# Kernel tuning notes

Measured on AMD Instinct MI355X. Metric: run time of the kernel, lower is better.

The kernel has to match this reference:

```python
import jax, jax.numpy as jnp
import numpy as np

B, L, W = 64, 20, 48
D = W * W           # 2304, MoE input/output size (image_width**2)
E = 4               # num_experts
HID = 2 * D         # expert hidden size
K = 1               # top_k
LOSS_COEF = 1e-2


def _cv_squared(x):
    # torch: x.var() (unbiased) / (x.mean()**2 + eps)
    eps = 1e-10
    return jnp.var(x, ddof=1) / (jnp.mean(x) ** 2 + eps)


def _moe(x, w_gate, w1, b1, w2, b2):
    # Noisy top-k gating, inference path (train=False => clean logits, no noise).
    logits = x @ w_gate                                   # [B, E]
    top_logits, top_idx = jax.lax.top_k(logits, K + 1)    # min(k+1, E)
    topk_gates = jax.nn.softmax(top_logits[:, :K], axis=-1)
    gates = jnp.zeros_like(logits).at[
        jnp.arange(x.shape[0])[:, None], top_idx[:, :K]
    ].set(topk_gates)                                     # [B, E] sparse gates
    importance = gates.sum(0)
    load = (gates > 0).sum(0).astype(x.dtype)             # _gates_to_load
    aux = LOSS_COEF * (_cv_squared(importance) + _cv_squared(load))
    # Dense expert compute weighted by gates (same math as dispatch/combine).
    h = jax.nn.relu(jnp.einsum('bd,edh->beh', x, w1) + b1)      # [B,E,HID]
    y = jnp.einsum('beh,ehd->bed', h, w2) + b2                  # [B,E,D]
    out = jnp.einsum('be,bed->bd', gates, y)                    # [B,D]
    return out, aux


def _conv3d(x, w, b, pad):
    y = jax.lax.conv_general_dilated(
        x, w, window_strides=(1, 1, 1), padding=pad,
        dimension_numbers=('NCDHW', 'OIDHW', 'NCDHW'))
    return y + b[None, :, None, None, None]


def _forward(input, conv1_w, conv1_b, conv2_w, conv2_b,
             t_gate, t_w1, t_b1, t_w2, t_b2,
             a_gate, a_w1, a_b1, a_w2, a_b2,
             q_gate, q_w1, q_b1, q_w2, q_b2,
             enc_w, enc_b, dec_w, dec_b):
    x = jnp.transpose(input, (0, 2, 1, 3, 4))                   # [B,1,L,H,W]
    x = jax.nn.relu(_conv3d(x, conv1_w, conv1_b, ((1, 1), (1, 1), (1, 1))))
    x = jax.nn.relu(_conv3d(x, conv2_w, conv2_b, ((0, 0), (1, 1), (1, 1))))  # [B,1,1,H,W]
    xf = x.reshape(x.shape[0], -1)                              # [B, D]
    transform, l1 = _moe(xf, t_gate, t_w1, t_b1, t_w2, t_b2)
    add, l2 = _moe(xf, a_gate, a_w1, a_b1, a_w2, a_b2)
    quad, l3 = _moe(xf, q_gate, q_w1, q_b1, q_w2, q_b2)
    s = input.shape                                             # [B,L,1,H,W]
    transform = transform.reshape(s[0], 1, s[2], s[3], s[4])
    add = add.reshape(s[0], 1, s[2], s[3], s[4])
    quad = quad.reshape(s[0], 1, s[2], s[3], s[4])
    out = input * input * quad + input * transform + add        # [B,L,1,H,W]
    # encoder = Linear(D,D)+ReLU, decoder = Linear(D,D) over flattened H*W
    of = out.reshape(s[0], s[1], D)
    of = jax.nn.relu(of @ enc_w + enc_b)
    of = of @ dec_w + dec_b
    of = jax.nn.sigmoid(of)
    return of.reshape(s), l1 + l2 + l3


def setup_inputs() -> dict:
    key = jax.random.key(0)
    ks = jax.random.split(key, 32)
    sc = 0.02
    inp = {
        'input': jax.random.normal(ks[0], (B, L, 1, W, W), jnp.float32),
        'conv1_w': jax.random.normal(ks[1], (10, 1, 3, 3, 3), jnp.float32) * sc,
        'conv1_b': jnp.zeros((10,), jnp.float32),
        'conv2_w': jax.random.normal(ks[2], (1, 10, L, 3, 3), jnp.float32) * sc,
        'conv2_b': jnp.zeros((1,), jnp.float32),
        'enc_w': jax.random.normal(ks[3], (D, D), jnp.float32) * sc,
        'enc_b': jnp.zeros((D,), jnp.float32),
        'dec_w': jax.random.normal(ks[4], (D, D), jnp.float32) * sc,
        'dec_b': jnp.zeros((D,), jnp.float32),
    }
    for i, p in enumerate(['t', 'a', 'q']):
        k0, k1, k2 = jax.random.split(ks[5 + i], 3)
        inp[p + '_gate'] = jnp.zeros((D, E), jnp.float32) + jax.random.normal(k0, (D, E), jnp.float32) * sc
        inp[p + '_w1'] = jax.random.normal(k1, (E, D, HID), jnp.float32) * sc
        inp[p + '_b1'] = jnp.zeros((E, HID), jnp.float32)
        inp[p + '_w2'] = jax.random.normal(k2, (E, HID, D), jnp.float32) * sc
        inp[p + '_b2'] = jnp.zeros((E, D), jnp.float32)
    return inp


def reference(input, conv1_w, conv1_b, conv2_w, conv2_b,
              t_gate, t_w1, t_b1, t_w2, t_b2,
              a_gate, a_w1, a_b1, a_w2, a_b2,
              q_gate, q_w1, q_b1, q_w2, q_b2,
              enc_w, enc_b, dec_w, dec_b):
    return _forward(input, conv1_w, conv1_b, conv2_w, conv2_b,
                    t_gate, t_w1, t_b1, t_w2, t_b2,
                    a_gate, a_w1, a_b1, a_w2, a_b2,
                    q_gate, q_w1, q_b1, q_w2, q_b2,
                    enc_w, enc_b, dec_w, dec_b)
```

## Files before the change

### kernel.cpp

```cpp
#include <hip/hip_runtime.h>
#include <stdint.h>

#define NB 64
#define NL 20
#define ND 2304
#define NE 4
#define NH 4608
#define NM 1280

typedef float f32x4 __attribute__((ext_vector_type(4)));
typedef __bf16 bf16x8 __attribute__((ext_vector_type(8)));
typedef unsigned short u16;
typedef u16 u16x4 __attribute__((ext_vector_type(4)));
typedef unsigned int u32;
typedef u32 u32x4 __attribute__((ext_vector_type(4)));

__device__ __forceinline__ u16 f2bf(float f) {
  u32 u = __builtin_bit_cast(u32, f);
  u += 0x7fffu + ((u >> 16) & 1u);
  return (u16)(u >> 16);
}

__device__ __forceinline__ void gl_lds16(const void* g, void* l) {
  __builtin_amdgcn_global_load_lds(
      (const __attribute__((address_space(1))) void*)g,
      (__attribute__((address_space(3))) void*)l, 16, 0, 0);
}

#define OFF_XFACC 0
#define OFF_XF    147456
#define OFF_H     294912
#define OFF_Y     1179648
#define OFF_AUX   1622016
#define OFF_CNT   1622020
#define OFF_ROWS  1622032
#define OFF_OFB   1622240
#define OFF_H1B   3096800
#define OFF_ENCWB 4571360
#define OFF_DECWB 7225568
#define OFF_XC    9879776
#define OFF_P     10322144

__global__ __launch_bounds__(256) void k_zero(float* __restrict__ p) {
  p[(size_t)blockIdx.x * 256 + threadIdx.x] = 0.f;
}

__global__ __launch_bounds__(256) void k_conv(
    const float* __restrict__ in, const float* __restrict__ w1,
    const float* __restrict__ b1, const float* __restrict__ w2,
    float* __restrict__ xf_acc) {
  __shared__ float insl[3][50][50];
  __shared__ float c1[2][50][50];
  __shared__ float w1s[270];
  __shared__ float w2s[90];
  __shared__ float b1s[10];
  const int d = blockIdx.x, b = blockIdx.y, t = threadIdx.x;
  for (int i = t; i < 270; i += 256) w1s[i] = w1[i];
  for (int i = t; i < 90; i += 256) w2s[i] = w2[(size_t)((i / 9) * 20 + d) * 9 + (i % 9)];
  if (t < 10) b1s[t] = b1[t];
  for (int i = t; i < 7500; i += 256) {
    int s = i / 2500, rr = (i % 2500) / 50, cc = i % 50;
    int gd = d - 1 + s, gy = rr - 1, gx = cc - 1;
    float v = 0.f;
    if (gd >= 0 && gd < NL && (unsigned)gy < 48u && (unsigned)gx < 48u)
      v = in[((size_t)b * NL + gd) * ND + gy * 48 + gx];
    insl[s][rr][cc] = v;
  }
  for (int i = t; i < 5000; i += 256) ((float*)c1)[i] = 0.f;
  float s2[3][4];
#pragma unroll
  for (int qi = 0; qi < 3; ++qi)
#pragma unroll
    for (int xq = 0; xq < 4; ++xq) s2[qi][xq] = 0.f;
  __syncthreads();
  for (int pc = 0; pc < 5; ++pc) {
#pragma unroll
    for (int qi = 0; qi < 3; ++qi) {
      int q = t + qi * 256;
      if (q < 576) {
        int y = q / 12, x0 = (q % 12) * 4;
        float a0[4], a1[4];
        const float bb0 = b1s[2 * pc], bb1 = b1s[2 * pc + 1];
#pragma unroll
        for (int xq = 0; xq < 4; ++xq) { a0[xq] = bb0; a1[xq] = bb1; }
#pragma unroll
        for (int kd = 0; kd < 3; ++kd)
#pragma unroll
          for (int ky = 0; ky < 3; ++ky) {
            float v[6];
#pragma unroll
            for (int i = 0; i < 6; ++i) v[i] = insl[kd][y + ky][x0 + i];
            const float* wa = &w1s[(2 * pc) * 27 + kd * 9 + ky * 3];
            const float* wb = wa + 27;
#pragma unroll
            for (int xq = 0; xq < 4; ++xq) {
              a0[xq] += v[xq] * wa[0] + v[xq + 1] * wa[1] + v[xq + 2] * wa[2];
              a1[xq] += v[xq] * wb[0] + v[xq + 1] * wb[1] + v[xq + 2] * wb[2];
            }
          }
#pragma unroll
        for (int xq = 0; xq < 4; ++xq) {
          c1[0][y + 1][x0 + 1 + xq] = fmaxf(a0[xq], 0.f);
          c1[1][y + 1][x0 + 1 + xq] = fmaxf(a1[xq], 0.f);
        }
      }
    }
    __syncthreads();
#pragma unroll
    for (int qi = 0; qi < 3; ++qi) {
      int q = t + qi * 256;
      if (q < 576) {
        int y = q / 12, x0 = (q % 12) * 4;
#pragma unroll
        for (int cc = 0; cc < 2; ++cc) {
#pragma unroll
          for (int ky = 0; ky < 3; ++ky) {
            float v[6];
#pragma unroll
            for (int i = 0; i < 6; ++i) v[i] = c1[cc][y + ky][x0 + i];
            const float* wr = &w2s[(2 * pc + cc) * 9 + ky * 3];
#pragma unroll
            for (int xq = 0; xq < 4; ++xq)
              s2[qi][xq] += v[xq] * wr[0] + v[xq + 1] * wr[1] + v[xq + 2] * wr[2];
          }
        }
      }
    }
    __syncthreads();
  }
#pragma unroll
  for (int qi = 0; qi < 3; ++qi) {
    int q = t + qi * 256;
    if (q < 576) {
#pragma unroll
      for (int xq = 0; xq < 4; ++xq)
        atomicAdd(&xf_acc[(size_t)b * ND + q * 4 + xq], s2[qi][xq]);
    }
  }
}

__global__ __launch_bounds__(256) void k_bias_relu(
    const float* __restrict__ acc, const float* __restrict__ c2b, float* __restrict__ xf) {
  size_t i = (size_t)blockIdx.x * 256 + threadIdx.x;
  xf[i] = fmaxf(acc[i] + c2b[0], 0.f);
}

__global__ __launch_bounds__(256) void k_gate(
    const float* __restrict__ xf,
    const float* __restrict__ g0, const float* __restrict__ g1, const float* __restrict__ g2,
    float* __restrict__ aux, int* __restrict__ cnt, int* __restrict__ rows) {
  const int p = blockIdx.x, t = threadIdx.x;
  const float* __restrict__ g = (p == 0) ? g0 : ((p == 1) ? g1 : g2);
  __shared__ float lg[64][4];
  __shared__ int lidx[64];
  __shared__ int lcnt[4];
  if (t < 4) lcnt[t] = 0;
  const int wv = t >> 6, l = t & 63;
  for (int b0 = 0; b0 < 64; b0 += 4) {
    int bb = b0 + wv;
    f32x4 acc = {0.f, 0.f, 0.f, 0.f};
    const float* xr = xf + (size_t)bb * ND + l * 36;
    const float* gr = g + (size_t)l * 36 * 4;
#pragma unroll
    for (int i4 = 0; i4 < 9; ++i4) {
      f32x4 xv = *(const f32x4*)(xr + i4 * 4);
#pragma unroll
      for (int qq = 0; qq < 4; ++qq) {
        f32x4 gv = *(const f32x4*)(gr + (i4 * 4 + qq) * 4);
        acc += xv[qq] * gv;
      }
    }
#pragma unroll
    for (int e = 0; e < 4; ++e) {
      float pv = acc[e];
#pragma unroll
      for (int off = 32; off > 0; off >>= 1) pv += __shfl_down(pv, off);
      if (l == 0) lg[bb][e] = pv;
    }
  }
  __syncthreads();
  if (t < 64) {
    float best = lg[t][0];
    int bi = 0;
#pragma unroll
    for (int e = 1; e < 4; ++e)
      if (lg[t][e] > best) { best = lg[t][e]; bi = e; }
    lidx[t] = bi;
    atomicAdd(&lcnt[bi], 1);
  }
  __syncthreads();
  if (t == 0) {
    int ofs[4]; int run = 0;
#pragma unroll
    for (int e = 0; e < 4; ++e) { ofs[e] = run; run += lcnt[e]; cnt[p * 4 + e] = lcnt[e]; }
    for (int b = 0; b < 64; ++b) { int e = lidx[b]; rows[p * 64 + ofs[e]++] = b; }
    float var = 0.f;
#pragma unroll
    for (int e = 0; e < 4; ++e) { float dd = (float)lcnt[e] - 16.f; var += dd * dd; }
    var *= (1.f / 3.f);
    aux[p] = 0.02f * var / (256.f + 1e-10f);
  }
}

__global__ __launch_bounds__(256) void k_gather(
    const float* __restrict__ xf, const int* __restrict__ rows, float* __restrict__ Xc) {
  const int slot = blockIdx.x, t = threadIdx.x;
  const int r = rows[slot];
  const f32x4* src = (const f32x4*)(xf + (size_t)r * ND);
  f32x4* dst = (f32x4*)(Xc + (size_t)slot * ND);
  for (int i = t; i < ND / 4; i += 256) dst[i] = src[i];
}

template <int K, int N, int KS>
__global__ __launch_bounds__(256) void k_moe_stream(
    const float* __restrict__ Xc,
    const float* __restrict__ wt, const float* __restrict__ wa, const float* __restrict__ wq,
    const int* __restrict__ cnt, float* __restrict__ P) {
  constexpr int KL = K / KS;
  constexpr int NT = KL / 32;
  const int tile = blockIdx.x;
  const int ks = blockIdx.y;
  const int pe = blockIdx.z >> 1, ch = blockIdx.z & 1;
  const int p = pe >> 2, e = pe & 3;
  const int c = cnt[p * 4 + e];
  const int rstart = ch * 32;
  if (rstart >= c) return;
  const int nrows = min(32, c - rstart);
  int pref = 0;
  for (int e2 = 0; e2 < e; ++e2) pref += cnt[p * 4 + e2];
  const int slot0 = p * 64 + pref + rstart;
  const float* __restrict__ W = (p == 0) ? wt : ((p == 1) ? wa : wq);
  __shared__ float xsb[2][32 * 32];
  __shared__ float wtb[2][32 * 128];
  const int t = threadIdx.x;
  const int w = t >> 6, l = t & 63;
  int slotc = slot0 + (t >> 3); if (slotc > 191) slotc = 191;
  const float* Xg = Xc + (size_t)slotc * K + ks * KL + (t & 7) * 4;
  const float* Wg = W + (size_t)e * K * N + (size_t)(ks * KL + (t >> 5)) * N
                      + tile * 128 + (t & 31) * 4;

#define STAGE(BUF, KT)                                                        \
  {                                                                           \
    const int k0_ = (KT) * 32;                                                \
    gl_lds16(Xg + k0_, &xsb[BUF][t * 4]);                                     \
    _Pragma("unroll")                                                         \
    for (int q = 0; q < 4; ++q)                                               \
      gl_lds16(Wg + (size_t)(k0_ + q * 8) * N, &wtb[BUF][q * 1024 + t * 4]);  \
  }

  float2 acc[8];
#pragma unroll
  for (int r = 0; r < 8; ++r) acc[r] = make_float2(0.f, 0.f);
  const int wrow = w * 8;
  const int colp = l * 2;

  STAGE(0, 0);
  asm volatile("s_waitcnt vmcnt(0)" ::: "memory");
  __syncthreads();

#pragma unroll 1
  for (int kt = 0; kt < NT; ++kt) {
    const int cur = kt & 1;
    if (kt + 1 < NT) STAGE(cur ^ 1, kt + 1);
    const float* xw = &xsb[cur][0];
    const float* ww = &wtb[cur][0];
#pragma unroll
    for (int k4 = 0; k4 < 8; ++k4) {
      float2 w0 = *(const float2*)(ww + (k4 * 4 + 0) * 128 + colp);
      float2 w1 = *(const float2*)(ww + (k4 * 4 + 1) * 128 + colp);
      float2 w2v = *(const float2*)(ww + (k4 * 4 + 2) * 128 + colp);
      float2 w3v = *(const float2*)(ww + (k4 * 4 + 3) * 128 + colp);
#pragma unroll
      for (int r = 0; r < 8; ++r) {
        f32x4 xv = *(const f32x4*)(xw + (wrow + r) * 32 + k4 * 4);
        acc[r].x = fmaf(xv[0], w0.x, acc[r].x);
        acc[r].y = fmaf(xv[0], w0.y, acc[r].y);
        acc[r].x = fmaf(xv[1], w1.x, acc[r].x);
        acc[r].y = fmaf(xv[1], w1.y, acc[r].y);
        acc[r].x = fmaf(xv[2], w2v.x, acc[r].x);
        acc[r].y = fmaf(xv[2], w2v.y, acc[r].y);
        acc[r].x = fmaf(xv[3], w3v.x, acc[r].x);
        acc[r].y = fmaf(xv[3], w3v.y, acc[r].y);
      }
    }
    asm volatile("s_waitcnt vmcnt(0)" ::: "memory");
    __syncthreads();
  }
#undef STAGE

  const size_t pbase = (size_t)ks * 192 * N;
#pragma unroll
  for (int r = 0; r < 8; ++r) {
    if (wrow + r < nrows)
      *(float2*)(P + pbase + (size_t)(slot0 + wrow + r) * N + tile * 128 + colp) = acc[r];
  }
}

__global__ __launch_bounds__(256) void k_red1(
    const float* __restrict__ P,
    const float* __restrict__ b1t, const float* __restrict__ b1a, const float* __restrict__ b1q,
    const int* __restrict__ cnt, float* __restrict__ H) {
  const int slot = blockIdx.y;
  const int p = slot >> 6, pos = slot & 63;
  int e = 0, run = cnt[p * 4];
  while (pos >= run && e < 3) { ++e; run += cnt[p * 4 + e]; }
  const float* __restrict__ b1 = (p == 0) ? b1t : ((p == 1) ? b1a : b1q);
  const int j0 = blockIdx.x * 1024 + threadIdx.x * 4;
  if (j0 >= NH) return;
  f32x4 s = *(const f32x4*)(b1 + (size_t)e * NH + j0);
#pragma unroll
  for (int ks = 0; ks < 8; ++ks)
    s += *(const f32x4*)(P + ((size_t)ks * 192 + slot) * NH + j0);
  f32x4 r;
#pragma unroll
  for (int q = 0; q < 4; ++q) r[q] = fmaxf(s[q], 0.f);
  *(f32x4*)(H + (size_t)slot * NH + j0) = r;
}

__global__ __launch_bounds__(256) void k_red2(
    const float* __restrict__ P,
    const float* __restrict__ b2t, const float* __restrict__ b2a, const float* __restrict__ b2q,
    const int* __restrict__ cnt, const int* __restrict__ rows, float* __restrict__ Y) {
  const int slot = blockIdx.y;
  const int p = slot >> 6, pos = slot & 63;
  int e = 0, run = cnt[p * 4];
  while (pos >= run && e < 3) { ++e; run += cnt[p * 4 + e]; }
  const float* __restrict__ b2 = (p == 0) ? b2t : ((p == 1) ? b2a : b2q);
  const int b = rows[slot];
  const int t = threadIdx.x;
  if (t >= 192) return;
  const int j0 = blockIdx.x * 768 + t * 4;
  f32x4 s = *(const f32x4*)(b2 + (size_t)e * ND + j0);
#pragma unroll
  for (int ks = 0; ks < 16; ++ks)
    s += *(const f32x4*)(P + ((size_t)ks * 192 + slot) * ND + j0);
  *(f32x4*)(Y + (size_t)(p * 64 + b) * ND + j0) = s;
}

__global__ __launch_bounds__(256) void k_combine(
    const float* __restrict__ in, const float* __restrict__ Y, u16* __restrict__ ofb) {
  const size_t i = (size_t)blockIdx.x * 256 + threadIdx.x;
  const size_t e0 = i * 4;
  const int row = (int)(e0 / ND);
  const int d = (int)(e0 - (size_t)row * ND);
  const int b = row / NL;
  f32x4 v = *(const f32x4*)(in + e0);
  const size_t yb = (size_t)b * ND + d;
  f32x4 tt = *(const f32x4*)(Y + yb);
  f32x4 aa = *(const f32x4*)(Y + (size_t)64 * ND + yb);
  f32x4 qq = *(const f32x4*)(Y + (size_t)128 * ND + yb);
  u16x4 o;
#pragma unroll
  for (int q = 0; q < 4; ++q) {
    float f = v[q] * v[q] * qq[q] + v[q] * tt[q] + aa[q];
    o[q] = f2bf(f);
  }
  *(u16x4*)(ofb + e0) = o;
}

__global__ __launch_bounds__(256) void k_wt(
    const float* __restrict__ encw, const float* __restrict__ decw,
    u16* __restrict__ encb, u16* __restrict__ decb) {
  __shared__ float tl[32][33];
  const float* __restrict__ src = blockIdx.z ? decw : encw;
  u16* __restrict__ dst = blockIdx.z ? decb : encb;
  const int k0 = blockIdx.x * 32, n0 = blockIdx.y * 32;
  const int tx = threadIdx.x & 31, ty = threadIdx.x >> 5;
  for (int r = ty; r < 32; r += 8) tl[r][tx] = src[(size_t)(k0 + r) * ND + n0 + tx];
  __syncthreads();
  for (int r = ty; r < 32; r += 8) dst[(size_t)(n0 + r) * ND + k0 + tx] = f2bf(tl[tx][r]);
}

template <int MODE>
__global__ __launch_bounds__(256) void k_gemm(
    const u16* __restrict__ A, const u16* __restrict__ Bt,
    const float* __restrict__ bias, void* __restrict__ outp,
    const float* __restrict__ aux) {
  __shared__ u16 As[128 * 32];
  __shared__ u16 Bs[128 * 32];
  const int t = threadIdx.x;
  const int bm = blockIdx.x, bn = blockIdx.y;
  const int lane = t & 63;
  const int wr = (t >> 7) & 1, wc = (t >> 6) & 1;
  const int l15 = lane & 15, l4 = lane >> 4;
  f32x4 acc[4][4] = {};
  const int r0 = t >> 2, kc0 = (t & 3) * 8;
  const int r1 = (t + 256) >> 2, kc1 = ((t + 256) & 3) * 8;
  const size_t baseA = (size_t)(bm * 128) * ND;
  const size_t baseB = (size_t)(bn * 128) * ND;
  for (int k0 = 0; k0 < ND; k0 += 32) {
    *(u32x4*)(As + t * 8) = *(const u32x4*)(A + baseA + (size_t)r0 * ND + k0 + kc0);
    *(u32x4*)(Bs + t * 8) = *(const u32x4*)(Bt + baseB + (size_t)r0 * ND + k0 + kc0);
    *(u32x4*)(As + (t + 256) * 8) = *(const u32x4*)(A + baseA + (size_t)r1 * ND + k0 + kc1);
    *(u32x4*)(Bs + (t + 256) * 8) = *(const u32x4*)(Bt + baseB + (size_t)r1 * ND + k0 + kc1);
    __syncthreads();
    bf16x8 af[4], bfr[4];
#pragma unroll
    for (int i = 0; i < 4; ++i) {
      af[i] = *(const bf16x8*)(As + (wr * 64 + i * 16 + l15) * 32 + l4 * 8);
      bfr[i] = *(const bf16x8*)(Bs + (wc * 64 + i * 16 + l15) * 32 + l4 * 8);
    }
#pragma unroll
    for (int mi = 0; mi < 4; ++mi)
#pragma unroll
      for (int ni = 0; ni < 4; ++ni)
        acc[mi][ni] = __builtin_amdgcn_mfma_f32_16x16x32_bf16(af[mi], bfr[ni], acc[mi][ni], 0, 0, 0);
    __syncthreads();
  }
  const int colbase = bn * 128 + wc * 64;
  const int rowbase = bm * 128 + wr * 64;
#pragma unroll
  for (int mi = 0; mi < 4; ++mi) {
#pragma unroll
    for (int ni = 0; ni < 4; ++ni) {
      const int colg = colbase + ni * 16 + l15;
      const float bv = bias[colg];
#pragma unroll
      for (int r = 0; r < 4; ++r) {
        const int rowg = rowbase + mi * 16 + l4 * 4 + r;
        float v = acc[mi][ni][r] + bv;
        if (MODE == 0) {
          ((u16*)outp)[(size_t)rowg * ND + colg] = f2bf(fmaxf(v, 0.f));
        } else {
          ((float*)outp)[(size_t)rowg * ND + colg] = 1.f / (1.f + __expf(-v));
        }
      }
    }
  }
  if (MODE == 1 && bm == 0 && bn == 0 && t == 0)
    ((float*)outp)[(size_t)NM * ND] = aux[0] + aux[1] + aux[2];
}

extern "C" void kernel_launch(void* const* d_in, const int* in_sizes, int n_in,
                              void* d_out, int out_size, void* d_ws, size_t ws_size,
                              hipStream_t stream) {
  (void)in_sizes; (void)n_in; (void)out_size; (void)ws_size;
  const float* input   = (const float*)d_in[0];
  const float* conv1_w = (const float*)d_in[1];
  const float* conv1_b = (const float*)d_in[2];
  const float* conv2_w = (const float*)d_in[3];
  const float* conv2_b = (const float*)d_in[4];
  const float* enc_w   = (const float*)d_in[5];
  const float* enc_b   = (const float*)d_in[6];
  const float* dec_w   = (const float*)d_in[7];
  const float* dec_b   = (const float*)d_in[8];
  const float* gate_t = (const float*)d_in[9];
  const float* w1_t   = (const float*)d_in[10];
  const float* b1_t   = (const float*)d_in[11];
  const float* w2_t   = (const float*)d_in[12];
  const float* b2_t   = (const float*)d_in[13];
  const float* gate_a = (const float*)d_in[14];
  const float* w1_a   = (const float*)d_in[15];
  const float* b1_a   = (const float*)d_in[16];
  const float* w2_a   = (const float*)d_in[17];
  const float* b2_a   = (const float*)d_in[18];
  const float* gate_q = (const float*)d_in[19];
  const float* w1_q   = (const float*)d_in[20];
  const float* b1_q   = (const float*)d_in[21];
  const float* w2_q   = (const float*)d_in[22];
  const float* b2_q   = (const float*)d_in[23];

  float* ws = (float*)d_ws;
  float* xf_acc = ws + OFF_XFACC;
  float* xf     = ws + OFF_XF;
  float* H      = ws + OFF_H;
  float* Y      = ws + OFF_Y;
  float* aux    = ws + OFF_AUX;
  int*   cnt    = (int*)(ws + OFF_CNT);
  int*   rows   = (int*)(ws + OFF_ROWS);
  u16*   ofb    = (u16*)(ws + OFF_OFB);
  u16*   h1b    = (u16*)(ws + OFF_H1B);
  u16*   encwb  = (u16*)(ws + OFF_ENCWB);
  u16*   decwb  = (u16*)(ws + OFF_DECWB);
  float* Xc     = ws + OFF_XC;
  float* P      = ws + OFF_P;

  k_zero<<<576, 256, 0, stream>>>(xf_acc);
  k_conv<<<dim3(20, 64), 256, 0, stream>>>(input, conv1_w, conv1_b, conv2_w, xf_acc);
  k_bias_relu<<<576, 256, 0, stream>>>(xf_acc, conv2_b, xf);
  k_wt<<<dim3(72, 72, 2), 256, 0, stream>>>(enc_w, dec_w, encwb, decwb);
  k_gate<<<3, 256, 0, stream>>>(xf, gate_t, gate_a, gate_q, aux, cnt, rows);
  k_gather<<<192, 256, 0, stream>>>(xf, rows, Xc);
  k_moe_stream<ND, NH, 8><<<dim3(36, 8, 24), 256, 0, stream>>>(Xc, w1_t, w1_a, w1_q, cnt, P);
  k_red1<<<dim3(5, 192), 256, 0, stream>>>(P, b1_t, b1_a, b1_q, cnt, H);
  k_moe_stream<NH, ND, 16><<<dim3(18, 16, 24), 256, 0, stream>>>(H, w2_t, w2_a, w2_q, cnt, P);
  k_red2<<<dim3(3, 192), 256, 0, stream>>>(P, b2_t, b2_a, b2_q, cnt, rows, Y);
  k_combine<<<2880, 256, 0, stream>>>(input, Y, ofb);
  k_gemm<0><<<dim3(10, 18), 256, 0, stream>>>(ofb, encwb, enc_b, (void*)h1b, aux);
  k_gemm<1><<<dim3(10, 18), 256, 0, stream>>>(h1b, decwb, dec_b, d_out, aux);
}
```

Before: 595.8 us.

## Halve MoE stream tile width and deepen LDS pipeline to triple buffering

The expert weight-streaming kernel now uses 64-column tiles instead of 128, doubling the grid so more workgroups keep HBM busy. LDS staging moves from double to triple buffering, with partial vmcnt waits so two stages of loads stay in flight while computing. Each thread now accumulates one column per row instead of two, which lowers register use but halves FMA work per LDS read of X. The X tile is reloaded twice as often in total, adding some redundant traffic.

After: 728.9 us. 22.3% more time.

```diff
diff --git a/kernel.cpp b/kernel.cpp
--- a/kernel.cpp
+++ b/kernel.cpp
@@ -230,61 +230,57 @@
   for (int e2 = 0; e2 < e; ++e2) pref += cnt[p * 4 + e2];
   const int slot0 = p * 64 + pref + rstart;
   const float* __restrict__ W = (p == 0) ? wt : ((p == 1) ? wa : wq);
-  __shared__ float xsb[2][32 * 32];
-  __shared__ float wtb[2][32 * 128];
+  __shared__ float xsb[3][32 * 32];
+  __shared__ float wtb[3][32 * 64];
   const int t = threadIdx.x;
   const int w = t >> 6, l = t & 63;
   int slotc = slot0 + (t >> 3); if (slotc > 191) slotc = 191;
   const float* Xg = Xc + (size_t)slotc * K + ks * KL + (t & 7) * 4;
-  const float* Wg = W + (size_t)e * K * N + (size_t)(ks * KL + (t >> 5)) * N
-                      + tile * 128 + (t & 31) * 4;
+  const float* Wg = W + (size_t)e * K * N + (size_t)(ks * KL + (t >> 4)) * N
+                      + tile * 64 + (t & 15) * 4;
 
 #define STAGE(BUF, KT)                                                        \
   {                                                                           \
     const int k0_ = (KT) * 32;                                                \
     gl_lds16(Xg + k0_, &xsb[BUF][t * 4]);                                     \
-    _Pragma("unroll")                                                         \
-    for (int q = 0; q < 4; ++q)                                               \
-      gl_lds16(Wg + (size_t)(k0_ + q * 8) * N, &wtb[BUF][q * 1024 + t * 4]);  \
-  }
-
-  float2 acc[8];
-#pragma unroll
-  for (int r = 0; r < 8; ++r) acc[r] = make_float2(0.f, 0.f);
+    gl_lds16(Wg + (size_t)k0_ * N, &wtb[BUF][t * 4]);                         \
+    gl_lds16(Wg + (size_t)(k0_ + 16) * N, &wtb[BUF][1024 + t * 4]);           \
+  }
+
+  float acc[8];
+#pragma unroll
+  for (int r = 0; r < 8; ++r) acc[r] = 0.f;
   const int wrow = w * 8;
-  const int colp = l * 2;
 
   STAGE(0, 0);
-  asm volatile("s_waitcnt vmcnt(0)" ::: "memory");
-  __syncthreads();
+  STAGE(1, 1);
 
 #pragma unroll 1
   for (int kt = 0; kt < NT; ++kt) {
-    const int cur = kt & 1;
-    if (kt + 1 < NT) STAGE(cur ^ 1, kt + 1);
-    const float* xw = &xsb[cur][0];
-    const float* ww = &wtb[cur][0];
+    if (kt < NT - 1) {
+      asm volatile("s_waitcnt vmcnt(3)" ::: "memory");
+    } else {
+      asm volatile("s_waitcnt vmcnt(0)" ::: "memory");
+    }
+    __syncthreads();
+    if (kt + 2 < NT) STAGE((kt + 2) % 3, kt + 2);
+    const float* xw = &xsb[kt % 3][0];
+    const float* ww = &wtb[kt % 3][0];
 #pragma unroll
     for (int k4 = 0; k4 < 8; ++k4) {
-      float2 w0 = *(const float2*)(ww + (k4 * 4 + 0) * 128 + colp);
-      float2 w1 = *(const float2*)(ww + (k4 * 4 + 1) * 128 + colp);
-      float2 w2v = *(const float2*)(ww + (k4 * 4 + 2) * 128 + colp);
-      float2 w3v = *(const float2*)(ww + (k4 * 4 + 3) * 128 + colp);
+      const float w0 = ww[(k4 * 4 + 0) * 64 + l];
+      const float w1v = ww[(k4 * 4 + 1) * 64 + l];
+      const float w2v = ww[(k4 * 4 + 2) * 64 + l];
+      const float w3v = ww[(k4 * 4 + 3) * 64 + l];
 #pragma unroll
       for (int r = 0; r < 8; ++r) {
         f32x4 xv = *(const f32x4*)(xw + (wrow + r) * 32 + k4 * 4);
-        acc[r].x = fmaf(xv[0], w0.x, acc[r].x);
-        acc[r].y = fmaf(xv[0], w0.y, acc[r].y);
-        acc[r].x = fmaf(xv[1], w1.x, acc[r].x);
-        acc[r].y = fmaf(xv[1], w1.y, acc[r].y);
-        acc[r].x = fmaf(xv[2], w2v.x, acc[r].x);
-        acc[r].y = fmaf(xv[2], w2v.y, acc[r].y);
-        acc[r].x = fmaf(xv[3], w3v.x, acc[r].x);
-        acc[r].y = fmaf(xv[3], w3v.y, acc[r].y);
+        acc[r] = fmaf(xv[0], w0, acc[r]);
+        acc[r] = fmaf(xv[1], w1v, acc[r]);
+        acc[r] = fmaf(xv[2], w2v, acc[r]);
+        acc[r] = fmaf(xv[3], w3v, acc[r]);
       }
     }
-    asm volatile("s_waitcnt vmcnt(0)" ::: "memory");
-    __syncthreads();
   }
 #undef STAGE
 
@@ -292,7 +288,7 @@
 #pragma unroll
   for (int r = 0; r < 8; ++r) {
     if (wrow + r < nrows)
-      *(float2*)(P + pbase + (size_t)(slot0 + wrow + r) * N + tile * 128 + colp) = acc[r];
+      P[pbase + (size_t)(slot0 + wrow + r) * N + tile * 64 + l] = acc[r];
   }
 }
 
@@ -481,9 +477,9 @@
   k_wt<<<dim3(72, 72, 2), 256, 0, stream>>>(enc_w, dec_w, encwb, decwb);
   k_gate<<<3, 256, 0, stream>>>(xf, gate_t, gate_a, gate_q, aux, cnt, rows);
   k_gather<<<192, 256, 0, stream>>>(xf, rows, Xc);
-  k_moe_stream<ND, NH, 8><<<dim3(36, 8, 24), 256, 0, stream>>>(Xc, w1_t, w1_a, w1_q, cnt, P);
+  k_moe_stream<ND, NH, 8><<<dim3(72, 8, 24), 256, 0, stream>>>(Xc, w1_t, w1_a, w1_q, cnt, P);
   k_red1<<<dim3(5, 192), 256, 0, stream>>>(P, b1_t, b1_a, b1_q, cnt, H);
-  k_moe_stream<NH, ND, 16><<<dim3(18, 16, 24), 256, 0, stream>>>(H, w2_t, w2_a, w2_q, cnt, P);
+  k_moe_stream<NH, ND, 16><<<dim3(36, 16, 24), 256, 0, stream>>>(H, w2_t, w2_a, w2_q, cnt, P);
   k_red2<<<dim3(3, 192), 256, 0, stream>>>(P, b2_t, b2_a, b2_q, cnt, rows, Y);
   k_combine<<<2880, 256, 0, stream>>>(input, Y, ofb);
   k_gemm<0><<<dim3(10, 18), 256, 0, stream>>>(ofb, encwb, enc_b, (void*)h1b, aux);
```
